# Performance work log

Measured on AMD Instinct MI355X. Metric: run time of the kernel, lower is better.

Reference implementation:

```python
import jax, jax.numpy as jnp
import numpy as np

KERNEL = 8
WEIGHT_INIT = np.array([0.49403, -0.44625, 0.82544, 0.99267, 1.6915, -2.0835, 2.9114,
                        -5.6555, 3.5984, -10.205, 20.828, -0.0022237, 0.0097854, 157.35],
                       dtype=np.float32)


def setup_inputs() -> dict:
    key = jax.random.key(0)
    x = jax.random.normal(key, (2048, 128, KERNEL, KERNEL), dtype=jnp.float32)
    weight = jnp.asarray(WEIGHT_INIT)
    return {"input": x, "weight": weight}


def reference(input, weight):
    eye = jnp.eye(KERNEL, dtype=input.dtype)  # serves as both mask and eye(8)
    # A = I - x @ x^T  over trailing two dims
    A = eye - jnp.matmul(input, jnp.swapaxes(input, 2, 3))
    B = jnp.matmul(A, A)
    C = jnp.matmul(B, A)
    D = jnp.matmul(C, A)
    E = jnp.matmul(D, A)
    F = jnp.matmul(E, A)
    G = jnp.matmul(F, A)
    Mat = (weight[0] * A + weight[1] * B + weight[2] * C + weight[3] * D
           + weight[4] * E + weight[5] * F + weight[6] * G + weight[7] * eye)
    return input + jnp.matmul(Mat, input)
```

## Files before the change

### kernel.cpp

```cpp
#include <hip/hip_runtime.h>


#define SE(p, q) S[(p) < (q) ? (p) : (q)][(p) < (q) ? (q) : (p)]
#define AE(p, q) A[(p) < (q) ? (p) : (q)][(p) < (q) ? (q) : (p)]
#define UT(M, p, q) M[(p) < (q) ? (p) : (q)][(p) < (q) ? (q) : (p)]
#define IN_T(p, q) ((q) < 4 || (p) + 4 <= (q))

__device__ __forceinline__ float pswap(float x)
{
    return __builtin_bit_cast(float,
        __builtin_amdgcn_update_dpp(0, __builtin_bit_cast(int, x),
                                    0xB1, 0xF, 0xF, true));
}

#define MAT_STEP(Pn, Po, wk)                                              \
    {                                                                     \
        _Pragma("unroll")                                                 \
        for (int p = 0; p < 8; ++p) {                                     \
            _Pragma("unroll")                                             \
            for (int q = p; q < 8; ++q) {                                 \
                if (IN_T(p, q)) {                                         \
                    float s = (p == q) ? (wk) : 0.0f;                     \
                    _Pragma("unroll")                                     \
                    for (int r = 0; r < 8; ++r)                           \
                        s += UT(Po, p, r) * AE(r, q);                     \
                    Pn[p][q] = s;                                         \
                }                                                         \
            }                                                             \
        }                                                                 \
        _Pragma("unroll")                                                 \
        for (int p = 0; p < 8; ++p) {                                     \
            _Pragma("unroll")                                             \
            for (int q = p; q < 8; ++q) {                                 \
                if (!IN_T(p, q)) {                                        \
                    const int pa = (p) ^ 4, pb = (q) ^ 4;                 \
                    const int lo = pa < pb ? pa : pb;                     \
                    const int hi = pa < pb ? pb : pa;                     \
                    Pn[p][q] = pswap(Pn[lo][hi]);                         \
                }                                                         \
            }                                                             \
        }                                                                 \
    }

__global__ __launch_bounds__(256, 2)
void ns_poly_kernel(const float* __restrict__ in,
                    const float* __restrict__ wp,
                    float* __restrict__ out)
{
    const int tid = threadIdx.x;
    const int m   = blockIdx.x * 128 + (tid >> 1);
    const int h   = tid & 1;

    const float w0 = wp[0], w1 = wp[1], w2 = wp[2], w3 = wp[3];
    const float w4 = wp[4], w5 = wp[5], w6 = wp[6], w7 = wp[7];

    const float* bp      = in + (size_t)m * 64 + h * 4;
    const float* baseOwn = bp + h * 32;
    const float* basePar = bp + (1 - h) * 32;

    float xc[4][8];
#pragma unroll
    for (int p = 0; p < 4; ++p) {
        const float4 v = *reinterpret_cast<const float4*>(baseOwn + p * 8);
        xc[0][p] = v.x; xc[1][p] = v.y; xc[2][p] = v.z; xc[3][p] = v.w;
    }
#pragma unroll
    for (int p = 0; p < 4; ++p) {
        const float4 v = *reinterpret_cast<const float4*>(basePar + p * 8);
        xc[0][4 + p] = v.x; xc[1][4 + p] = v.y; xc[2][4 + p] = v.z; xc[3][4 + p] = v.w;
    }

    float S[8][8];
#pragma unroll
    for (int p = 0; p < 8; ++p)
#pragma unroll
        for (int q = p; q < 8; ++q) {
            float s = xc[0][p] * xc[0][q];
            s += xc[1][p] * xc[1][q];
            s += xc[2][p] * xc[2][q];
            s += xc[3][p] * xc[3][q];
            S[p][q] = s;
        }

    float A[8][8];
#pragma unroll
    for (int p = 0; p < 8; ++p)
#pragma unroll
        for (int q = p; q < 8; ++q) {
            const float other = pswap(SE((p) ^ 4, (q) ^ 4));
            A[p][q] = (p == q ? 1.0f : 0.0f) - S[p][q] - other;
        }

    float P[8][8], Q[8][8];
#pragma unroll
    for (int p = 0; p < 8; ++p)
#pragma unroll
        for (int q = p; q < 8; ++q)
            P[p][q] = (p == q) ? fmaf(w6, A[p][q], w5) : w6 * A[p][q];

    MAT_STEP(Q, P, w4);
    MAT_STEP(P, Q, w3);
    MAT_STEP(Q, P, w2);
    MAT_STEP(P, Q, w1);
    MAT_STEP(Q, P, w0);
    MAT_STEP(P, Q, 1.0f + w7);

    float t[4][8];
#pragma unroll
    for (int jj = 0; jj < 4; ++jj)
#pragma unroll
        for (int p = 0; p < 8; ++p) {
            float s = UT(P, p, 0) * xc[jj][0];
#pragma unroll
            for (int q = 1; q < 8; ++q)
                s += UT(P, p, q) * xc[jj][q];
            t[jj][p] = s;
        }

    float* obp     = out + (size_t)m * 64 + h * 4;
    float* oandOwn = obp + h * 32;
    float* oandPar = obp + (1 - h) * 32;
#pragma unroll
    for (int p = 0; p < 4; ++p)
        *reinterpret_cast<float4*>(oandOwn + p * 8) =
            make_float4(t[0][p], t[1][p], t[2][p], t[3][p]);
#pragma unroll
    for (int p = 0; p < 4; ++p)
        *reinterpret_cast<float4*>(oandPar + p * 8) =
            make_float4(t[0][4 + p], t[1][4 + p], t[2][4 + p], t[3][4 + p]);
}

extern "C" void kernel_launch(void* const* d_in, const int* in_sizes, int n_in,
                              void* d_out, int out_size, void* d_ws, size_t ws_size,
                              hipStream_t stream)
{
    const float* in = (const float*)d_in[0];
    const float* w  = (const float*)d_in[1];
    float* outp     = (float*)d_out;

    const int nmat   = in_sizes[0] / 64;
    const int blocks = nmat / 128;
    ns_poly_kernel<<<blocks, 256, 0, stream>>>(in, w, outp);
}
```

Baseline: 123.5 us.

## Stage input and output through swizzled LDS with packed FP32 Gram computation

Input tiles are loaded per wave straight into LDS with global_load_lds, using an XOR-swizzled layout. The output is staged back through LDS before fully coalesced float4 stores. This replaces the old strided per-thread float4 global accesses, and the input is re-read from LDS after the polynomial steps instead of being held in registers across them. The Gram product now uses v_pk_mul/v_pk_fma packed FP32. The change adds 32KB of LDS per block, which may limit occupancy, and relies on wave-local sync through waitcnt only.

```diff
diff --git a/kernel.cpp b/kernel.cpp
--- a/kernel.cpp
+++ b/kernel.cpp
@@ -1,10 +1,16 @@
 #include <hip/hip_runtime.h>
 
 
-#define SE(p, q) S[(p) < (q) ? (p) : (q)][(p) < (q) ? (q) : (p)]
-#define AE(p, q) A[(p) < (q) ? (p) : (q)][(p) < (q) ? (q) : (p)]
-#define UT(M, p, q) M[(p) < (q) ? (p) : (q)][(p) < (q) ? (q) : (p)]
-#define IN_T(p, q) ((q) < 4 || (p) + 4 <= (q))
+typedef float v2f __attribute__((ext_vector_type(2)));
+
+__device__ __forceinline__ v2f pk_mul(v2f a, v2f b) {
+    v2f d;
+    asm("v_pk_mul_f32 %0, %1, %2" : "=v"(d) : "v"(a), "v"(b));
+    return d;
+}
+__device__ __forceinline__ void pk_fma(v2f &acc, v2f a, v2f b) {
+    asm("v_pk_fma_f32 %0, %1, %2, %0" : "+v"(acc) : "v"(a), "v"(b));
+}
 
 __device__ __forceinline__ float pswap(float x)
 {
@@ -12,6 +18,16 @@
         __builtin_amdgcn_update_dpp(0, __builtin_bit_cast(int, x),
                                     0xB1, 0xF, 0xF, true));
 }
+
+#define GLOAD_LDS16(gp, lp)                                               \
+    __builtin_amdgcn_global_load_lds(                                     \
+        (const __attribute__((address_space(1))) void*)(gp),              \
+        (__attribute__((address_space(3))) void*)(lp), 16, 0, 0)
+
+#define SE(p, q) S[(p) < (q) ? (p) : (q)][(p) < (q) ? (q) : (p)]
+#define AE(p, q) A[(p) < (q) ? (p) : (q)][(p) < (q) ? (q) : (p)]
+#define UT(M, p, q) M[(p) < (q) ? (p) : (q)][(p) < (q) ? (q) : (p)]
+#define IN_T(p, q) ((q) < 4 || (p) + 4 <= (q))
 
 #define MAT_STEP(Pn, Po, wk)                                              \
     {                                                                     \
@@ -47,27 +63,41 @@
                     const float* __restrict__ wp,
                     float* __restrict__ out)
 {
-    const int tid = threadIdx.x;
-    const int m   = blockIdx.x * 128 + (tid >> 1);
-    const int h   = tid & 1;
+    __shared__ float4 lds[2048];
+
+    const int tid  = threadIdx.x;
+    const int wave = tid >> 6;
+    const int lane = tid & 63;
+    const int l    = lane >> 1;
+    const int h    = lane & 1;
 
     const float w0 = wp[0], w1 = wp[1], w2 = wp[2], w3 = wp[3];
     const float w4 = wp[4], w5 = wp[5], w6 = wp[6], w7 = wp[7];
 
-    const float* bp      = in + (size_t)m * 64 + h * 4;
-    const float* baseOwn = bp + h * 32;
-    const float* basePar = bp + (1 - h) * 32;
+    float4* L = lds + wave * 512;
 
-    float xc[4][8];
+    const size_t base =
+        ((size_t)blockIdx.x * 128 + (size_t)wave * 32) * 16;
+    const float4* __restrict__ gin  = reinterpret_cast<const float4*>(in);
+    float4*       __restrict__ gout = reinterpret_cast<float4*>(out);
+
 #pragma unroll
-    for (int p = 0; p < 4; ++p) {
-        const float4 v = *reinterpret_cast<const float4*>(baseOwn + p * 8);
-        xc[0][p] = v.x; xc[1][p] = v.y; xc[2][p] = v.z; xc[3][p] = v.w;
+    for (int it = 0; it < 8; ++it) {
+        const int C = it * 64 + lane;
+        const int Cs = C ^ (((C >> 4) & 3) << 1);
+        GLOAD_LDS16(gin + base + Cs, L + it * 64);
     }
+    asm volatile("s_waitcnt vmcnt(0)" ::: "memory");
+    __builtin_amdgcn_sched_barrier(0);
+
+    v2f y[2][8];
 #pragma unroll
-    for (int p = 0; p < 4; ++p) {
-        const float4 v = *reinterpret_cast<const float4*>(basePar + p * 8);
-        xc[0][4 + p] = v.x; xc[1][4 + p] = v.y; xc[2][4 + p] = v.z; xc[3][4 + p] = v.w;
+    for (int p = 0; p < 8; ++p) {
+        const int rr = (p < 4) ? (4 * h + p) : (4 * (1 - h) + (p - 4));
+        const int f4 = (l * 16 + rr * 2 + h) ^ ((l & 3) << 1);
+        const float4 v = L[f4];
+        y[0][p] = (v2f){v.x, v.y};
+        y[1][p] = (v2f){v.z, v.w};
     }
 
     float S[8][8];
@@ -75,11 +105,9 @@
     for (int p = 0; p < 8; ++p)
 #pragma unroll
         for (int q = p; q < 8; ++q) {
-            float s = xc[0][p] * xc[0][q];
-            s += xc[1][p] * xc[1][q];
-            s += xc[2][p] * xc[2][q];
-            s += xc[3][p] * xc[3][q];
-            S[p][q] = s;
+            v2f a = pk_mul(y[0][p], y[0][q]);
+            pk_fma(a, y[1][p], y[1][q]);
+            S[p][q] = a.x + a.y;
         }
 
     float A[8][8];
@@ -105,29 +133,41 @@
     MAT_STEP(Q, P, w0);
     MAT_STEP(P, Q, 1.0f + w7);
 
+    v2f z[2][8];
+#pragma unroll
+    for (int p = 0; p < 8; ++p) {
+        const int rr = (p < 4) ? (4 * h + p) : (4 * (1 - h) + (p - 4));
+        const int f4 = (l * 16 + rr * 2 + h) ^ ((l & 3) << 1);
+        const float4 v = L[f4];
+        z[0][p] = (v2f){v.x, v.y};
+        z[1][p] = (v2f){v.z, v.w};
+    }
+
     float t[4][8];
 #pragma unroll
     for (int jj = 0; jj < 4; ++jj)
 #pragma unroll
         for (int p = 0; p < 8; ++p) {
-            float s = UT(P, p, 0) * xc[jj][0];
+            float s = UT(P, p, 0) * z[jj >> 1][0][jj & 1];
 #pragma unroll
             for (int q = 1; q < 8; ++q)
-                s += UT(P, p, q) * xc[jj][q];
+                s += UT(P, p, q) * z[jj >> 1][q][jj & 1];
             t[jj][p] = s;
         }
 
-    float* obp     = out + (size_t)m * 64 + h * 4;
-    float* oandOwn = obp + h * 32;
-    float* oandPar = obp + (1 - h) * 32;
 #pragma unroll
-    for (int p = 0; p < 4; ++p)
-        *reinterpret_cast<float4*>(oandOwn + p * 8) =
-            make_float4(t[0][p], t[1][p], t[2][p], t[3][p]);
+    for (int p = 0; p < 8; ++p) {
+        const int rr = (p < 4) ? (4 * h + p) : (4 * (1 - h) + (p - 4));
+        const int f4 = (l * 16 + rr * 2 + h) ^ ((l & 3) << 1);
+        L[f4] = make_float4(t[0][p], t[1][p], t[2][p], t[3][p]);
+    }
+    asm volatile("s_waitcnt lgkmcnt(0)" ::: "memory");
+
 #pragma unroll
-    for (int p = 0; p < 4; ++p)
-        *reinterpret_cast<float4*>(oandPar + p * 8) =
-            make_float4(t[0][4 + p], t[1][4 + p], t[2][4 + p], t[3][4 + p]);
+    for (int it = 0; it < 8; ++it) {
+        const int C = it * 64 + lane;
+        gout[base + C] = L[C ^ (((C >> 4) & 3) << 1)];
+    }
 }
 
 extern "C" void kernel_launch(void* const* d_in, const int* in_sizes, int n_in,
```

After: 123.0 us. Within noise of the previous version (-0.3%).
